# Optimization experiments

Measured on AMD Instinct MI355X. Metric: run time of the kernel, lower is better.

## Reference

```python
import jax, jax.numpy as jnp
import numpy as np

# dims
B, N, T, F, D = 16, 64, 168, 8, 248   # batch, stations, seq, features, gcn_dim
E = D + F                              # transformer dmodel = 256
H = 8                                  # attention heads
FF = 4 * E                             # expansion_factor * dmodel


def _layer_norm(x, g, b, eps=1e-5):
    m = jnp.mean(x, axis=-1, keepdims=True)
    v = jnp.var(x, axis=-1, keepdims=True)
    return (x - m) * jax.lax.rsqrt(v + eps) * g + b


def setup_inputs() -> dict:
    key = jax.random.key(0)
    ks = jax.random.split(key, 20)
    s = 0.02
    return {
        'x': jax.random.normal(ks[0], (B, N, T, F), jnp.float32),
        'locs': jax.random.uniform(ks[1], (B, N, 2), jnp.float32),
        'pos_em': jax.random.normal(ks[2], (B, T, E), jnp.float32),
        'periodic_em': jax.random.normal(ks[3], (B, T, E), jnp.float32),
        'gcn_w': jax.random.normal(ks[4], (F, D), jnp.float32) * s,
        'gcn_b': jnp.zeros((D,), jnp.float32),
        'fc1_w': jax.random.normal(ks[5], (D, D), jnp.float32) * s,
        'fc1_b': jnp.zeros((D,), jnp.float32),
        'wq': jax.random.normal(ks[6], (E, E), jnp.float32) * s,
        'bq': jnp.zeros((E,), jnp.float32),
        'wk': jax.random.normal(ks[7], (E, E), jnp.float32) * s,
        'bk': jnp.zeros((E,), jnp.float32),
        'wv': jax.random.normal(ks[8], (E, E), jnp.float32) * s,
        'bv': jnp.zeros((E,), jnp.float32),
        'wo': jax.random.normal(ks[9], (E, E), jnp.float32) * s,
        'bo': jnp.zeros((E,), jnp.float32),
        'ln1_g': jnp.ones((E,), jnp.float32),
        'ln1_b': jnp.zeros((E,), jnp.float32),
        'ln2_g': jnp.ones((E,), jnp.float32),
        'ln2_b': jnp.zeros((E,), jnp.float32),
        'ff1_w': jax.random.normal(ks[10], (E, FF), jnp.float32) * s,
        'ff1_b': jnp.zeros((FF,), jnp.float32),
        'ff2_w': jax.random.normal(ks[11], (FF, E), jnp.float32) * s,
        'ff2_b': jnp.zeros((E,), jnp.float32),
    }


def reference(x, locs, pos_em, periodic_em, gcn_w, gcn_b, fc1_w, fc1_b,
              wq, bq, wk, bk, wv, bv, wo, bo,
              ln1_g, ln1_b, ln2_g, ln2_b, ff1_w, ff1_b, ff2_w, ff2_b):
    b, n, t, f = x.shape
    # --- inverse-distance-weighted dense adjacency (fully connected graph) ---
    diff = locs[:, :, None, :] - locs[:, None, :, :]            # [B,N,N,2]
    dist = jnp.sqrt(jnp.sum(diff * diff, -1) + 1e-12)           # [B,N,N]
    w = jnp.where(jnp.eye(n, dtype=bool), 0.0, 1.0 / dist)      # no self edges
    w = w / jnp.sum(w, -1, keepdims=True)                       # norm=True
    # --- GCNConv (self loops + symmetric normalization), batched over B and T ---
    a = w + jnp.eye(n, dtype=x.dtype)
    dinv = jax.lax.rsqrt(jnp.sum(a, -1))
    a = a * dinv[:, :, None] * dinv[:, None, :]                 # [B,N,N]
    h = jnp.einsum('bntf,fd->bntd', x, gcn_w)                   # xW
    g = jax.nn.relu(jnp.einsum('bmn,bntd->bmtd', a, h) + gcn_b) # aggregate + relu
    g = jnp.einsum('bntd,de->bnte', g, fc1_w) + fc1_b           # fc1
    # --- concat features, flatten stations into batch, add positional embedding ---
    tok = jnp.concatenate([x, g], -1).reshape(b * n, t, -1)     # [B*N,T,E]
    tok = tok + jnp.repeat(pos_em, n, axis=0)                   # dropout=identity (eval)
    per = jnp.repeat(periodic_em, n, axis=0)
    # --- transformer encoder layer (periodic embedding conditions Q/K) ---
    e = tok.shape[-1]
    dh = e // H
    qk_in = tok + per
    q = (qk_in @ wq + bq).reshape(b * n, t, H, dh)
    k = (qk_in @ wk + bk).reshape(b * n, t, H, dh)
    v = (tok @ wv + bv).reshape(b * n, t, H, dh)
    s = jnp.einsum('bthd,bshd->bhts', q, k) * (1.0 / float(np.sqrt(dh)))
    p = jax.nn.softmax(s, axis=-1)
    o = jnp.einsum('bhts,bshd->bthd', p, v).reshape(b * n, t, e)
    o = o @ wo + bo
    h1 = _layer_norm(tok + o, ln1_g, ln1_b)
    ff = jax.nn.relu(h1 @ ff1_w + ff1_b) @ ff2_w + ff2_b
    out = _layer_norm(h1 + ff, ln2_g, ln2_b)
    return out.reshape(b, n, t, e)
```

## Files before the change

### kernel.cpp

```cpp
#include <hip/hip_runtime.h>
#include <hip/hip_bf16.h>

constexpr int B_  = 16;
constexpr int N_  = 64;
constexpr int T_  = 168;
constexpr int F_  = 8;
constexpr int E_  = 256;
constexpr int H_  = 8;
constexpr int DH_ = 32;
constexpr int NT_ = N_ * T_;
constexpr int LDQ_ = 768;

typedef __bf16 bf16x8 __attribute__((ext_vector_type(8)));
typedef float  f32x4  __attribute__((ext_vector_type(4)));
typedef float  f32x4u __attribute__((ext_vector_type(4), aligned(4)));

__device__ __forceinline__ unsigned short f2b(float f) {
  union { float f; unsigned int u; } v; v.f = f;
  unsigned int r = (v.u + 0x7FFFu + ((v.u >> 16) & 1u)) >> 16;
  return (unsigned short)r;
}
__device__ __forceinline__ float b2f(unsigned short h) {
  union { unsigned int u; float f; } v; v.u = ((unsigned int)h) << 16;
  return v.f;
}
__device__ __forceinline__ unsigned int cvtpk(float lo, float hi) {
  unsigned int r;
  asm("v_cvt_pk_bf16_f32 %0, %1, %2" : "=v"(r) : "v"(lo), "v"(hi));
  return r;
}
__device__ __forceinline__ void gload16(const void* g, void* l) {
  __builtin_amdgcn_global_load_lds(
      (const __attribute__((address_space(1))) unsigned int*)g,
      (__attribute__((address_space(3))) unsigned int*)l, 16, 0, 0);
}

__global__ void adj_kernel(const float* __restrict__ locs, float* __restrict__ a) {
  int b = blockIdx.x;
  int m = threadIdx.x;
  __shared__ float lx[64], ly[64];
  lx[m] = locs[(b * 64 + m) * 2 + 0];
  ly[m] = locs[(b * 64 + m) * 2 + 1];
  __syncthreads();
  float x = lx[m], y = ly[m];
  float sum = 0.f;
  for (int n = 0; n < 64; ++n) {
    float dx = x - lx[n], dy = y - ly[n];
    float d = sqrtf(dx * dx + dy * dy + 1e-12f);
    sum += (n == m) ? 0.f : 1.f / d;
  }
  float inv = 0.5f / sum;
  for (int n = 0; n < 64; ++n) {
    float dx = x - lx[n], dy = y - ly[n];
    float d = sqrtf(dx * dx + dy * dy + 1e-12f);
    float w = (n == m) ? 0.5f : inv / d;
    a[(b * 64 + m) * 64 + n] = w;
  }
}

__global__ void convw_kernel(const float* __restrict__ in, unsigned short* __restrict__ outT,
                             int K, int N, int Kp, int Np) {
  int idx = blockIdx.x * 256 + threadIdx.x;
  if (idx >= Np * Kp) return;
  int n = idx / Kp, k = idx % Kp;
  float v = (k < K && n < N) ? in[(long)k * N + n] : 0.f;
  outT[idx] = f2b(v);
}

__global__ __launch_bounds__(256) void gcn_kernel(
    const float* __restrict__ x, const float* __restrict__ adj,
    const float* __restrict__ gcn_w, const float* __restrict__ gcn_b,
    const float* __restrict__ pos_em, const float* __restrict__ per_em,
    unsigned short* __restrict__ G, unsigned short* __restrict__ tokb,
    unsigned short* __restrict__ qkb, int b0) {
  int bl = blockIdx.x / T_;
  int t = blockIdx.x % T_;
  int b = b0 + bl;
  int tid = threadIdx.x;
  __shared__ float sX[512];
  __shared__ float sXA[512];
  const float* adjb = adj + b * 4096;
  for (int i = tid; i < 512; i += 256) {
    int n = i >> 3, f = i & 7;
    sX[i] = x[((long)(b * 64 + n) * T_ + t) * F_ + f];
  }
  __syncthreads();
  for (int i = tid; i < 512; i += 256) {
    int m = i >> 3, f = i & 7;
    float s = 0.f;
    for (int n = 0; n < 64; ++n) s += adjb[(m << 6) + n] * sX[(n << 3) + f];
    sXA[i] = s;
  }
  {
    long pbase = ((long)bl * T_ + t) * E_;
    for (int i = tid; i < 512; i += 256) {
      int m = i >> 3, f = i & 7;
      long lrow = (long)(bl * 64 + m) * T_ + t;
      float base = sX[i] + pos_em[pbase + f];
      tokb[lrow * E_ + f] = f2b(base);
      qkb[lrow * E_ + f]  = f2b(base + per_em[pbase + f]);
    }
  }
  __syncthreads();
  for (int i = tid; i < 64 * 256; i += 256) {
    int m = i >> 8, d = i & 255;
    float v = 0.f;
    if (d < 248) {
      float s = gcn_b[d];
      const float* xam = &sXA[m << 3];
#pragma unroll
      for (int f = 0; f < 8; ++f) s += xam[f] * gcn_w[f * 248 + d];
      v = fmaxf(s, 0.f);
    }
    long lrow = (long)(bl * 64 + m) * T_ + t;
    G[lrow * 256 + d] = f2b(v);
  }
}

template <int KCHUNKS, int WAVES>
__global__ __launch_bounds__(WAVES * 64) void block_gemm(
    const unsigned short* __restrict__ A, int lda,
    const unsigned short* __restrict__ Bt, int K, int Nact,
    const float* __restrict__ bias,
    float* Cf, unsigned short* Cb1, unsigned short* Cb2,
    const float* __restrict__ emb1, const float* __restrict__ emb2,
    const unsigned short* __restrict__ resb, const float* resf,
    int c0, int ldc, int relu) {
  __shared__ unsigned short As[64 * 256];
  const int tid = threadIdx.x;
  const int lane = tid & 63, w = tid >> 6;
  const int l15 = lane & 15, lg = lane >> 4;
  const int m0 = blockIdx.x * 64;
  const int n0w = blockIdx.y * (WAVES * 64) + w * 64;

  f32x4 acc[4][4];
#pragma unroll
  for (int i = 0; i < 4; ++i)
#pragma unroll
    for (int j = 0; j < 4; ++j) acc[i][j] = (f32x4){0.f, 0.f, 0.f, 0.f};

  for (int kc = 0; kc < KCHUNKS; ++kc) {
    if (kc) __syncthreads();
#pragma unroll
    for (int j = 0; j < 32 / WAVES; ++j) {
      int idx = j * (WAVES * 64) + tid;
      int row = idx >> 5, g = idx & 31;
      int swg = (g & 24) | ((g & 7) ^ (row & 7));
      gload16(A + (long)(m0 + row) * lda + kc * 256 + swg * 8,
              &As[(j * (WAVES * 64) + w * 64) * 8]);
    }
    bf16x8 Wa[4], Wb[4], Xf[4];
    auto ldw = [&](bf16x8 (&W)[4], int ks) {
#pragma unroll
      for (int nf = 0; nf < 4; ++nf)
        W[nf] = *reinterpret_cast<const bf16x8*>(
            Bt + (long)(n0w + nf * 16 + l15) * K + kc * 256 + ks * 32 + (lg << 3));
    };
    auto ldx = [&](int ks) {
#pragma unroll
      for (int mf = 0; mf < 4; ++mf) {
        int row = (mf << 4) + l15;
        int ksg = (ks << 2) + lg;
        int sw = (ksg & 24) | ((ksg & 7) ^ (row & 7));
        Xf[mf] = *reinterpret_cast<const bf16x8*>(&As[((row << 5) + sw) * 8]);
      }
    };
    auto mm = [&](bf16x8 (&W)[4]) {
      __builtin_amdgcn_s_setprio(1);
#pragma unroll
      for (int mf = 0; mf < 4; ++mf)
#pragma unroll
        for (int nf = 0; nf < 4; ++nf)
          acc[mf][nf] = __builtin_amdgcn_mfma_f32_16x16x32_bf16(W[nf], Xf[mf], acc[mf][nf], 0, 0, 0);
      __builtin_amdgcn_s_setprio(0);
    };
    ldw(Wa, 0);
    asm volatile("s_waitcnt vmcnt(0)" ::: "memory");
    __syncthreads();
#pragma unroll
    for (int kp = 0; kp < 4; ++kp) {
      ldw(Wb, kp * 2 + 1);
      ldx(kp * 2);
      mm(Wa);
      if (kp < 3) ldw(Wa, kp * 2 + 2);
      ldx(kp * 2 + 1);
      mm(Wb);
    }
  }

  const int cb = lg << 2;
#pragma unroll
  for (int mf = 0; mf < 4; ++mf) {
    int rr = m0 + (mf << 4) + l15;
    int ar = (rr / NT_) * T_ + (rr % T_);
    long rbase  = (long)rr * ldc + c0;
    long rbase2 = (long)rr * 256 + c0;
    long abase  = (long)ar * 256 + c0;
#pragma unroll
    for (int nf = 0; nf < 4; ++nf) {
      int gcol = n0w + (nf << 4) + cb;
      if (gcol < Nact) {
        float v0 = acc[mf][nf][0], v1 = acc[mf][nf][1];
        float v2 = acc[mf][nf][2], v3 = acc[mf][nf][3];
        if (bias) {
          f32x4u b4 = *reinterpret_cast<const f32x4u*>(bias + gcol);
          v0 += b4[0]; v1 += b4[1]; v2 += b4[2]; v3 += b4[3];
        }
        if (relu) {
          v0 = fmaxf(v0, 0.f); v1 = fmaxf(v1, 0.f);
          v2 = fmaxf(v2, 0.f); v3 = fmaxf(v3, 0.f);
        }
        if (resb) {
          ushort4 rv = *reinterpret_cast<const ushort4*>(resb + rbase2 + gcol);
          v0 += b2f(rv.x); v1 += b2f(rv.y); v2 += b2f(rv.z); v3 += b2f(rv.w);
        }
        if (resf) {
          f32x4u r4 = *reinterpret_cast<const f32x4u*>(resf + rbase + gcol);
          v0 += r4[0]; v1 += r4[1]; v2 += r4[2]; v3 += r4[3];
        }
        if (emb1) {
          f32x4u e4 = *reinterpret_cast<const f32x4u*>(emb1 + abase + gcol);
          v0 += e4[0]; v1 += e4[1]; v2 += e4[2]; v3 += e4[3];
        }
        if (Cf) {
          f32x4u o; o[0] = v0; o[1] = v1; o[2] = v2; o[3] = v3;
          *reinterpret_cast<f32x4u*>(Cf + rbase + gcol) = o;
        }
        if (Cb1) {
          uint2 p = {cvtpk(v0, v1), cvtpk(v2, v3)};
          *reinterpret_cast<uint2*>(Cb1 + rbase + gcol) = p;
        }
        if (Cb2) {
          f32x4u e4 = *reinterpret_cast<const f32x4u*>(emb2 + abase + gcol);
          uint2 p = {cvtpk(v0 + e4[0], v1 + e4[1]), cvtpk(v2 + e4[2], v3 + e4[3])};
          *reinterpret_cast<uint2*>(Cb2 + rbase + gcol) = p;
        }
      }
    }
  }
}

__global__ __launch_bounds__(256) void wo_ln_kernel(
    const unsigned short* __restrict__ A, int lda,
    const unsigned short* __restrict__ Wt,
    const float* __restrict__ bias,
    const unsigned short* __restrict__ resb,
    const float* __restrict__ lng, const float* __restrict__ lnb,
    unsigned short* __restrict__ outb) {
  __shared__ unsigned short As[64 * 256];
  __shared__ float red[4][4][16][2];
  const int tid = threadIdx.x;
  const int lane = tid & 63, w = tid >> 6;
  const int l15 = lane & 15, lg = lane >> 4;
  const int m0 = blockIdx.x * 64;
  const int n0w = w * 64;

  f32x4 acc[4][4];
#pragma unroll
  for (int i = 0; i < 4; ++i)
#pragma unroll
    for (int j = 0; j < 4; ++j) acc[i][j] = (f32x4){0.f, 0.f, 0.f, 0.f};

#pragma unroll
  for (int j = 0; j < 8; ++j) {
    int idx = j * 256 + tid;
    int row = idx >> 5, g = idx & 31;
    int swg = (g & 24) | ((g & 7) ^ (row & 7));
    gload16(A + (long)(m0 + row) * lda + swg * 8, &As[(j * 256 + w * 64) * 8]);
  }
  bf16x8 Wa[4], Wb[4], Xf[4];
  auto ldw = [&](bf16x8 (&W)[4], int ks) {
#pragma unroll
    for (int nf = 0; nf < 4; ++nf)
      W[nf] = *reinterpret_cast<const bf16x8*>(
          Wt + (long)(n0w + nf * 16 + l15) * 256 + ks * 32 + (lg << 3));
  };
  auto ldx = [&](int ks) {
#pragma unroll
    for (int mf = 0; mf < 4; ++mf) {
      int row = (mf << 4) + l15;
      int ksg = (ks << 2) + lg;
      int sw = (ksg & 24) | ((ksg & 7) ^ (row & 7));
      Xf[mf] = *reinterpret_cast<const bf16x8*>(&As[((row << 5) + sw) * 8]);
    }
  };
  auto mm = [&](bf16x8 (&W)[4]) {
    __builtin_amdgcn_s_setprio(1);
#pragma unroll
    for (int mf = 0; mf < 4; ++mf)
#pragma unroll
      for (int nf = 0; nf < 4; ++nf)
        acc[mf][nf] = __builtin_amdgcn_mfma_f32_16x16x32_bf16(W[nf], Xf[mf], acc[mf][nf], 0, 0, 0);
    __builtin_amdgcn_s_setprio(0);
  };
  ldw(Wa, 0);
  asm volatile("s_waitcnt vmcnt(0)" ::: "memory");
  __syncthreads();
#pragma unroll
  for (int kp = 0; kp < 4; ++kp) {
    ldw(Wb, kp * 2 + 1);
    ldx(kp * 2);
    mm(Wa);
    if (kp < 3) ldw(Wa, kp * 2 + 2);
    ldx(kp * 2 + 1);
    mm(Wb);
  }

  const int cb = lg << 2;
  float s[4], s2[4];
#pragma unroll
  for (int mf = 0; mf < 4; ++mf) {
    int rr = m0 + (mf << 4) + l15;
    long rbase2 = (long)rr * 256;
    s[mf] = 0.f; s2[mf] = 0.f;
#pragma unroll
    for (int nf = 0; nf < 4; ++nf) {
      int gcol = n0w + (nf << 4) + cb;
      f32x4u b4 = *reinterpret_cast<const f32x4u*>(bias + gcol);
      ushort4 rv = *reinterpret_cast<const ushort4*>(resb + rbase2 + gcol);
      float v0 = acc[mf][nf][0] + b4[0] + b2f(rv.x);
      float v1 = acc[mf][nf][1] + b4[1] + b2f(rv.y);
      float v2 = acc[mf][nf][2] + b4[2] + b2f(rv.z);
      float v3 = acc[mf][nf][3] + b4[3] + b2f(rv.w);
      acc[mf][nf][0] = v0; acc[mf][nf][1] = v1;
      acc[mf][nf][2] = v2; acc[mf][nf][3] = v3;
      s[mf] += v0 + v1 + v2 + v3;
      s2[mf] += v0 * v0 + v1 * v1 + v2 * v2 + v3 * v3;
    }
    s[mf] += __shfl_xor(s[mf], 16, 64);
    s[mf] += __shfl_xor(s[mf], 32, 64);
    s2[mf] += __shfl_xor(s2[mf], 16, 64);
    s2[mf] += __shfl_xor(s2[mf], 32, 64);
    if (lg == 0) { red[w][mf][l15][0] = s[mf]; red[w][mf][l15][1] = s2[mf]; }
  }
  __syncthreads();
#pragma unroll
  for (int mf = 0; mf < 4; ++mf) {
    float S  = red[0][mf][l15][0] + red[1][mf][l15][0] + red[2][mf][l15][0] + red[3][mf][l15][0];
    float S2 = red[0][mf][l15][1] + red[1][mf][l15][1] + red[2][mf][l15][1] + red[3][mf][l15][1];
    float mean = S * 0.00390625f;
    float var = S2 * 0.00390625f - mean * mean;
    float rs = rsqrtf(var + 1e-5f);
    int rr = m0 + (mf << 4) + l15;
    long rbase = (long)rr * 256;
#pragma unroll
    for (int nf = 0; nf < 4; ++nf) {
      int gcol = n0w + (nf << 4) + cb;
      f32x4u g4 = *reinterpret_cast<const f32x4u*>(lng + gcol);
      f32x4u t4 = *reinterpret_cast<const f32x4u*>(lnb + gcol);
      float o0 = (acc[mf][nf][0] - mean) * rs * g4[0] + t4[0];
      float o1 = (acc[mf][nf][1] - mean) * rs * g4[1] + t4[1];
      float o2 = (acc[mf][nf][2] - mean) * rs * g4[2] + t4[2];
      float o3 = (acc[mf][nf][3] - mean) * rs * g4[3] + t4[3];
      uint2 p = {cvtpk(o0, o1), cvtpk(o2, o3)};
      *reinterpret_cast<uint2*>(outb + rbase + gcol) = p;
    }
  }
}

__global__ __launch_bounds__(512, 4) void ff_fused_kernel(
    const unsigned short* __restrict__ h1,
    const unsigned short* __restrict__ W1,
    const unsigned short* __restrict__ W2,
    const float* __restrict__ b1, const float* __restrict__ b2,
    const float* __restrict__ lng, const float* __restrict__ lnb,
    float* __restrict__ out) {
  __shared__ unsigned short h1s[64 * 256];
  __shared__ unsigned short fisA[64 * 128];
  __shared__ unsigned short fisB[64 * 128];
  __shared__ float red[8][4][16][2];
  const int tid = threadIdx.x;
  const int lane = tid & 63, w = tid >> 6;
  const int l15 = lane & 15, lg = lane >> 4;
  const int m0 = blockIdx.x * 64;
  const int cb = lg << 2;

#pragma unroll
  for (int j = 0; j < 4; ++j) {
    int idx = j * 512 + tid;
    int row = idx >> 5, g = idx & 31;
    int swg = (g & 24) | ((g & 7) ^ (row & 7));
    gload16(h1 + (long)(m0 + row) * 256 + swg * 8, &h1s[(j * 512 + w * 64) * 8]);
  }
  asm volatile("s_waitcnt vmcnt(0)" ::: "memory");
  __syncthreads();

  f32x4 acc2[4][2];
#pragma unroll
  for (int i = 0; i < 4; ++i)
#pragma unroll
    for (int j = 0; j < 2; ++j) acc2[i][j] = (f32x4){0.f, 0.f, 0.f, 0.f};

  auto ldw1 = [&](bf16x8& W, int hc, int ks) {
    W = *reinterpret_cast<const bf16x8*>(
        W1 + (long)(hc * 128 + w * 16 + l15) * 256 + ks * 32 + (lg << 3));
  };
  auto stage1 = [&](f32x4 (&a1)[4], int hc) {
#pragma unroll
    for (int i = 0; i < 4; ++i) a1[i] = (f32x4){0.f, 0.f, 0.f, 0.f};
    bf16x8 Wa, Wb, Xf[4];
    auto ldxh = [&](int ks) {
#pragma unroll
      for (int mf = 0; mf < 4; ++mf) {
        int row = (mf << 4) + l15;
        int ksg = (ks << 2) + lg;
        int sw = (ksg & 24) | ((ksg & 7) ^ (row & 7));
        Xf[mf] = *reinterpret_cast<const bf16x8*>(&h1s[((row << 5) + sw) * 8]);
      }
    };
    ldw1(Wa, hc, 0);
#pragma unroll
    for (int kp = 0; kp < 4; ++kp) {
      ldw1(Wb, hc, kp * 2 + 1);
      ldxh(kp * 2);
      __builtin_amdgcn_s_setprio(1);
#pragma unroll
      for (int mf = 0; mf < 4; ++mf)
        a1[mf] = __builtin_amdgcn_mfma_f32_16x16x32_bf16(Wa, Xf[mf], a1[mf], 0, 0, 0);
      __builtin_amdgcn_s_setprio(0);
      if (kp < 3) ldw1(Wa, hc, kp * 2 + 2);
      ldxh(kp * 2 + 1);
      __builtin_amdgcn_s_setprio(1);
#pragma unroll
      for (int mf = 0; mf < 4; ++mf)
        a1[mf] = __builtin_amdgcn_mfma_f32_16x16x32_bf16(Wb, Xf[mf], a1[mf], 0, 0, 0);
      __builtin_amdgcn_s_setprio(0);
    }
  };
  auto stage2 = [&](const unsigned short* fis, int hc) {
    bf16x8 Wf[2], Xf[4];
#pragma unroll
    for (int ks = 0; ks < 4; ++ks) {
#pragma unroll
      for (int nf = 0; nf < 2; ++nf)
        Wf[nf] = *reinterpret_cast<const bf16x8*>(
            W2 + (long)(w * 32 + nf * 16 + l15) * 1024 + hc * 128 + ks * 32 + (lg << 3));
#pragma unroll
      for (int mf = 0; mf < 4; ++mf) {
        int row = (mf << 4) + l15;
        int ksg = (ks << 2) + lg;
        int sw = (ksg & 8) | ((ksg & 7) ^ (row & 7));
        Xf[mf] = *reinterpret_cast<const bf16x8*>(&fis[((row << 4) + sw) * 8]);
      }
      __builtin_amdgcn_s_setprio(1);
#pragma unroll
      for (int mf = 0; mf < 4; ++mf)
#pragma unroll
        for (int nf = 0; nf < 2; ++nf)
          acc2[mf][nf] = __builtin_amdgcn_mfma_f32_16x16x32_bf16(Wf[nf], Xf[mf], acc2[mf][nf], 0, 0, 0);
      __builtin_amdgcn_s_setprio(0);
    }
  };
  auto writeFis = [&](unsigned short* fis, f32x4 (&a1)[4], int hc) {
    int col = w * 16 + cb;
    f32x4u b4 = *reinterpret_cast<const f32x4u*>(b1 + hc * 128 + col);
    int g = col >> 3;
#pragma unroll
    for (int mf = 0; mf < 4; ++mf) {
      int row = (mf << 4) + l15;
      float v0 = fmaxf(a1[mf][0] + b4[0], 0.f);
      float v1 = fmaxf(a1[mf][1] + b4[1], 0.f);
      float v2 = fmaxf(a1[mf][2] + b4[2], 0.f);
      float v3 = fmaxf(a1[mf][3] + b4[3], 0.f);
      int swg = (g & 8) | ((g & 7) ^ (row & 7));
      uint2 p = {cvtpk(v0, v1), cvtpk(v2, v3)};
      *reinterpret_cast<uint2*>(&fis[((row << 4) + swg) * 8 + (col & 7)]) = p;
    }
  };

  f32x4 a1[4];
  stage1(a1, 0);
  writeFis(fisA, a1, 0);
  __syncthreads();

#pragma unroll
  for (int hc = 0; hc < 8; ++hc) {
    const unsigned short* rdp = (hc & 1) ? fisB : fisA;
    unsigned short* wrp = (hc & 1) ? fisA : fisB;
    if (hc < 7) stage1(a1, hc + 1);
    stage2(rdp, hc);
    if (hc < 7) {
      writeFis(wrp, a1, hc + 1);
      __syncthreads();
    }
  }

  float s[4], s2[4];
#pragma unroll
  for (int mf = 0; mf < 4; ++mf) {
    int row = (mf << 4) + l15;
    s[mf] = 0.f; s2[mf] = 0.f;
#pragma unroll
    for (int nf = 0; nf < 2; ++nf) {
      int gcol = w * 32 + (nf << 4) + cb;
      f32x4u b4 = *reinterpret_cast<const f32x4u*>(b2 + gcol);
      int g = gcol >> 3;
      int swg = (g & 24) | ((g & 7) ^ (row & 7));
      ushort4 rv = *reinterpret_cast<const ushort4*>(&h1s[((row << 5) + swg) * 8 + (gcol & 7)]);
      float v0 = acc2[mf][nf][0] + b4[0] + b2f(rv.x);
      float v1 = acc2[mf][nf][1] + b4[1] + b2f(rv.y);
      float v2 = acc2[mf][nf][2] + b4[2] + b2f(rv.z);
      float v3 = acc2[mf][nf][3] + b4[3] + b2f(rv.w);
      acc2[mf][nf][0] = v0; acc2[mf][nf][1] = v1;
      acc2[mf][nf][2] = v2; acc2[mf][nf][3] = v3;
      s[mf] += v0 + v1 + v2 + v3;
      s2[mf] += v0 * v0 + v1 * v1 + v2 * v2 + v3 * v3;
    }
    s[mf] += __shfl_xor(s[mf], 16, 64);
    s[mf] += __shfl_xor(s[mf], 32, 64);
    s2[mf] += __shfl_xor(s2[mf], 16, 64);
    s2[mf] += __shfl_xor(s2[mf], 32, 64);
    if (lg == 0) { red[w][mf][l15][0] = s[mf]; red[w][mf][l15][1] = s2[mf]; }
  }
  __syncthreads();
#pragma unroll
  for (int mf = 0; mf < 4; ++mf) {
    float S = 0.f, S2 = 0.f;
#pragma unroll
    for (int ww = 0; ww < 8; ++ww) { S += red[ww][mf][l15][0]; S2 += red[ww][mf][l15][1]; }
    float mean = S * 0.00390625f;
    float var = S2 * 0.00390625f - mean * mean;
    float rs = rsqrtf(var + 1e-5f);
    int rr = m0 + (mf << 4) + l15;
    long rbase = (long)rr * 256;
#pragma unroll
    for (int nf = 0; nf < 2; ++nf) {
      int gcol = w * 32 + (nf << 4) + cb;
      f32x4u g4 = *reinterpret_cast<const f32x4u*>(lng + gcol);
      f32x4u t4 = *reinterpret_cast<const f32x4u*>(lnb + gcol);
      f32x4u o;
      o[0] = (acc2[mf][nf][0] - mean) * rs * g4[0] + t4[0];
      o[1] = (acc2[mf][nf][1] - mean) * rs * g4[1] + t4[1];
      o[2] = (acc2[mf][nf][2] - mean) * rs * g4[2] + t4[2];
      o[3] = (acc2[mf][nf][3] - mean) * rs * g4[3] + t4[3];
      *reinterpret_cast<f32x4u*>(out + rbase + gcol) = o;
    }
  }
}

__global__ __launch_bounds__(256) void attn_mfma_kernel(unsigned short* QKV) {
  int blk = blockIdx.x;
  int bn = blk >> 3, h = blk & 7;
  int tid = threadIdx.x;
  int lane = tid & 63, w = tid >> 6;

  __shared__ unsigned short Kfr[11 * 512];
  __shared__ unsigned short VT[32][200];
  __shared__ unsigned short Pb[4][16][200];

  const long qbase = (long)bn * T_ * LDQ_ + h * DH_;
  const unsigned short* Kg = QKV + qbase + 256;
  const unsigned short* V  = QKV + qbase + 512;
  const unsigned short* Q  = QKV + qbase;
  unsigned short* O = QKV + qbase;
  int l15 = lane & 15, lg = lane >> 4;

  for (int kt = w; kt < 11; kt += 4) {
    gload16(Kg + (long)(kt * 16 + l15) * LDQ_ + (lg << 3), &Kfr[kt * 512]);
  }
  for (int i = tid; i < T_ * 4; i += 256) {
    int t = i >> 2, seg = (i & 3) << 3;
    uint4 vv = *reinterpret_cast<const uint4*>(V + (long)t * LDQ_ + seg);
    const unsigned short* vs = (const unsigned short*)&vv;
#pragma unroll
    for (int j = 0; j < 8; ++j) VT[seg + j][t] = vs[j];
  }
  for (int i = tid; i < 32 * 32; i += 256) VT[i >> 5][168 + (i & 31)] = 0;
  {
    unsigned short* pflat = &Pb[0][0][0];
    for (int i = tid; i < 64 * 24; i += 256)
      pflat[(i / 24) * 200 + 176 + (i % 24)] = 0;
  }
  __syncthreads();

  const float scale = 0.17677669529663687f;
  unsigned short* Pw = &Pb[w][0][0];

  for (int it = 0; it < 3; ++it) {
    int qt = w + it * 4;
    if (qt > 10) break;
    bf16x8 af = *reinterpret_cast<const bf16x8*>(
        Q + (long)(qt * 16 + l15) * LDQ_ + (lg << 3));
    f32x4 s[11];
#pragma unroll
    for (int kt = 0; kt < 11; ++kt) {
      bf16x8 bf = *reinterpret_cast<const bf16x8*>(&Kfr[kt * 512 + lane * 8]);
      s[kt] = __builtin_amdgcn_mfma_f32_16x16x32_bf16(
          af, bf, (f32x4){0.f, 0.f, 0.f, 0.f}, 0, 0, 0);
    }
    bool ok10 = (l15 < 8);
    float inv_l[4];
#pragma unroll
    for (int r = 0; r < 4; ++r) {
      float mx = -1e30f;
#pragma unroll
      for (int kt = 0; kt < 10; ++kt) mx = fmaxf(mx, s[kt][r] * scale);
      if (ok10) mx = fmaxf(mx, s[10][r] * scale);
#pragma unroll
      for (int off = 1; off < 16; off <<= 1) mx = fmaxf(mx, __shfl_xor(mx, off, 64));
      float pv[11];
      float ls = 0.f;
#pragma unroll
      for (int kt = 0; kt < 11; ++kt) {
        bool valid = (kt < 10) || ok10;
        float p = valid ? __expf(s[kt][r] * scale - mx) : 0.f;
        pv[kt] = p;
        ls += p;
      }
#pragma unroll
      for (int off = 1; off < 16; off <<= 1) ls += __shfl_xor(ls, off, 64);
      inv_l[r] = 1.f / ls;
      int prow = (lg << 2) + r;
#pragma unroll
      for (int kt = 0; kt < 11; ++kt)
        Pw[prow * 200 + kt * 16 + l15] = f2b(pv[kt]);
    }
    asm volatile("s_waitcnt lgkmcnt(0)" ::: "memory");
    __builtin_amdgcn_sched_barrier(0);
    f32x4 o0 = (f32x4){0.f, 0.f, 0.f, 0.f};
    f32x4 o1 = (f32x4){0.f, 0.f, 0.f, 0.f};
#pragma unroll
    for (int ks = 0; ks < 6; ++ks) {
      bf16x8 pf = *reinterpret_cast<const bf16x8*>(&Pw[l15 * 200 + ks * 32 + (lg << 3)]);
      bf16x8 v0 = *reinterpret_cast<const bf16x8*>(&VT[l15][ks * 32 + (lg << 3)]);
      bf16x8 v1 = *reinterpret_cast<const bf16x8*>(&VT[16 + l15][ks * 32 + (lg << 3)]);
      o0 = __builtin_amdgcn_mfma_f32_16x16x32_bf16(pf, v0, o0, 0, 0, 0);
      o1 = __builtin_amdgcn_mfma_f32_16x16x32_bf16(pf, v1, o1, 0, 0, 0);
    }
    int rg = lg << 2;
#pragma unroll
    for (int r = 0; r < 4; ++r) {
      int q = qt * 16 + rg + r;
      if (q < T_) {
        long ob = (long)q * LDQ_;
        O[ob + l15]      = f2b(o0[r] * inv_l[r]);
        O[ob + 16 + l15] = f2b(o1[r] * inv_l[r]);
      }
    }
  }
}

extern "C" void kernel_launch(void* const* d_in, const int* in_sizes, int n_in,
                              void* d_out, int out_size, void* d_ws, size_t ws_size,
                              hipStream_t stream) {
  const float* x      = (const float*)d_in[0];
  const float* locs   = (const float*)d_in[1];
  const float* pos_em = (const float*)d_in[2];
  const float* per_em = (const float*)d_in[3];
  const float* gcn_w  = (const float*)d_in[4];
  const float* gcn_b  = (const float*)d_in[5];
  const float* fc1_w  = (const float*)d_in[6];
  const float* fc1_b  = (const float*)d_in[7];
  const float* wq = (const float*)d_in[8];
  const float* bq = (const float*)d_in[9];
  const float* wk = (const float*)d_in[10];
  const float* bk = (const float*)d_in[11];
  const float* wv = (const float*)d_in[12];
  const float* bv = (const float*)d_in[13];
  const float* wo = (const float*)d_in[14];
  const float* bo = (const float*)d_in[15];
  const float* ln1_g = (const float*)d_in[16];
  const float* ln1_b = (const float*)d_in[17];
  const float* ln2_g = (const float*)d_in[18];
  const float* ln2_b = (const float*)d_in[19];
  const float* ff1_w = (const float*)d_in[20];
  const float* ff1_b = (const float*)d_in[21];
  const float* ff2_w = (const float*)d_in[22];
  const float* ff2_b = (const float*)d_in[23];
  float* out = (float*)d_out;

  const size_t ADJ_BYTES = 1u << 20;
  const size_t WB_BYTES  = 2u << 20;
  int CB = 16;
  while (CB > 1) {
    if (ADJ_BYTES + WB_BYTES + (size_t)CB * NT_ * 2560 <= ws_size) break;
    CB >>= 1;
  }
  char* ws = (char*)d_ws;
  float* adj = (float*)ws;
  unsigned short* wslab = (unsigned short*)(ws + ADJ_BYTES);
  unsigned short* fc1T  = wslab;
  unsigned short* wqkT  = wslab + 65536;
  unsigned short* wkT   = wslab + 2 * 65536;
  unsigned short* wvT   = wslab + 3 * 65536;
  unsigned short* woT   = wslab + 4 * 65536;
  unsigned short* ff1T  = wslab + 5 * 65536;
  unsigned short* ff2T  = wslab + 5 * 65536 + 262144;
  float* bqk = (float*)(ws + ADJ_BYTES + 1900544);

  unsigned short* tokb = (unsigned short*)(ws + ADJ_BYTES + WB_BYTES);
  unsigned short* qkb  = tokb + (size_t)CB * NT_ * 256;
  unsigned short* qkv  = qkb + (size_t)CB * NT_ * 256;
  unsigned short* h1b  = tokb;

  adj_kernel<<<B_, 64, 0, stream>>>(locs, adj);
  convw_kernel<<<256, 256, 0, stream>>>(fc1_w, fc1T, 248, 248, 256, 256);
  convw_kernel<<<256, 256, 0, stream>>>(wq, wqkT, 256, 256, 256, 256);
  convw_kernel<<<256, 256, 0, stream>>>(wk, wkT, 256, 256, 256, 256);
  convw_kernel<<<256, 256, 0, stream>>>(wv, wvT, 256, 256, 256, 256);
  convw_kernel<<<256, 256, 0, stream>>>(wo, woT, 256, 256, 256, 256);
  convw_kernel<<<1024, 256, 0, stream>>>(ff1_w, ff1T, 256, 1024, 256, 1024);
  convw_kernel<<<1024, 256, 0, stream>>>(ff2_w, ff2T, 1024, 256, 1024, 256);
  hipMemcpyAsync(bqk, bq, 256 * sizeof(float), hipMemcpyDeviceToDevice, stream);
  hipMemcpyAsync(bqk + 256, bk, 256 * sizeof(float), hipMemcpyDeviceToDevice, stream);

  for (int b0 = 0; b0 < B_; b0 += CB) {
    const int rows = CB * NT_;
    const int GX = rows / 64;
    const float* pos_c = pos_em + (long)b0 * T_ * E_;
    const float* per_c = per_em + (long)b0 * T_ * E_;
    float* out_c = out + (long)b0 * NT_ * E_;
    unsigned short* G = qkv;

    gcn_kernel<<<CB * T_, 256, 0, stream>>>(x, adj, gcn_w, gcn_b, pos_c, per_c,
                                            G, tokb, qkb, b0);
    block_gemm<1, 4><<<dim3(GX, 1), 256, 0, stream>>>(
        G, 256, fc1T, 256, 248, fc1_b, nullptr, tokb, qkb, pos_c, per_c,
        nullptr, nullptr, 8, 256, 0);
    block_gemm<1, 8><<<dim3(GX, 1), 512, 0, stream>>>(
        qkb, 256, wqkT, 256, 512, bqk, nullptr, qkv, nullptr, nullptr, nullptr,
        nullptr, nullptr, 0, LDQ_, 0);
    block_gemm<1, 4><<<dim3(GX, 1), 256, 0, stream>>>(
        tokb, 256, wvT, 256, 256, bv, nullptr, qkv, nullptr, nullptr, nullptr,
        nullptr, nullptr, 512, LDQ_, 0);
    attn_mfma_kernel<<<CB * N_ * H_, 256, 0, stream>>>(qkv);
    wo_ln_kernel<<<GX, 256, 0, stream>>>(qkv, LDQ_, woT, bo, tokb,
                                         ln1_g, ln1_b, h1b);
    ff_fused_kernel<<<GX, 512, 0, stream>>>(h1b, ff1T, ff2T, ff1_b, ff2_b,
                                            ln2_g, ln2_b, out_c);
  }
}
```

Before: 1.173 ms.

## Restructure fused FFN to single fis buffer with register-prefetched W1/W2 weights

```diff
diff --git a/kernel.cpp b/kernel.cpp
--- a/kernel.cpp
+++ b/kernel.cpp
@@ -366,8 +366,7 @@
     const float* __restrict__ lng, const float* __restrict__ lnb,
     float* __restrict__ out) {
   __shared__ unsigned short h1s[64 * 256];
-  __shared__ unsigned short fisA[64 * 128];
-  __shared__ unsigned short fisB[64 * 128];
+  __shared__ unsigned short fis[64 * 128];
   __shared__ float red[8][4][16][2];
   const int tid = threadIdx.x;
   const int lane = tid & 63, w = tid >> 6;
@@ -382,8 +381,6 @@
     int swg = (g & 24) | ((g & 7) ^ (row & 7));
     gload16(h1 + (long)(m0 + row) * 256 + swg * 8, &h1s[(j * 512 + w * 64) * 8]);
   }
-  asm volatile("s_waitcnt vmcnt(0)" ::: "memory");
-  __syncthreads();
 
   f32x4 acc2[4][2];
 #pragma unroll
@@ -391,98 +388,97 @@
 #pragma unroll
     for (int j = 0; j < 2; ++j) acc2[i][j] = (f32x4){0.f, 0.f, 0.f, 0.f};
 
+  bf16x8 W1all[8], W2A[2], W2B[2], Xf[4];
   auto ldw1 = [&](bf16x8& W, int hc, int ks) {
     W = *reinterpret_cast<const bf16x8*>(
         W1 + (long)(hc * 128 + w * 16 + l15) * 256 + ks * 32 + (lg << 3));
   };
-  auto stage1 = [&](f32x4 (&a1)[4], int hc) {
+  auto ldw2 = [&](bf16x8 (&W)[2], int hc, int ks) {
+#pragma unroll
+    for (int nf = 0; nf < 2; ++nf)
+      W[nf] = *reinterpret_cast<const bf16x8*>(
+          W2 + (long)(w * 32 + nf * 16 + l15) * 1024 + hc * 128 + ks * 32 + (lg << 3));
+  };
+  auto ldxh = [&](int ks) {
+#pragma unroll
+    for (int mf = 0; mf < 4; ++mf) {
+      int row = (mf << 4) + l15;
+      int ksg = (ks << 2) + lg;
+      int sw = (ksg & 24) | ((ksg & 7) ^ (row & 7));
+      Xf[mf] = *reinterpret_cast<const bf16x8*>(&h1s[((row << 5) + sw) * 8]);
+    }
+  };
+  auto ldxf = [&](int ks) {
+#pragma unroll
+    for (int mf = 0; mf < 4; ++mf) {
+      int row = (mf << 4) + l15;
+      int ksg = (ks << 2) + lg;
+      int sw = (ksg & 8) | ((ksg & 7) ^ (row & 7));
+      Xf[mf] = *reinterpret_cast<const bf16x8*>(&fis[((row << 4) + sw) * 8]);
+    }
+  };
+  auto mm2 = [&](bf16x8 (&W)[2]) {
+    __builtin_amdgcn_s_setprio(1);
+#pragma unroll
+    for (int mf = 0; mf < 4; ++mf)
+#pragma unroll
+      for (int nf = 0; nf < 2; ++nf)
+        acc2[mf][nf] = __builtin_amdgcn_mfma_f32_16x16x32_bf16(W[nf], Xf[mf], acc2[mf][nf], 0, 0, 0);
+    __builtin_amdgcn_s_setprio(0);
+  };
+
+#pragma unroll
+  for (int ks = 0; ks < 8; ++ks) ldw1(W1all[ks], 0, ks);
+  asm volatile("s_waitcnt vmcnt(8)" ::: "memory");
+  __syncthreads();
+
+  for (int hc = 0; hc < 8; ++hc) {
+    f32x4 a1[4];
 #pragma unroll
     for (int i = 0; i < 4; ++i) a1[i] = (f32x4){0.f, 0.f, 0.f, 0.f};
-    bf16x8 Wa, Wb, Xf[4];
-    auto ldxh = [&](int ks) {
+    ldw2(W2A, hc, 0);
+    ldw2(W2B, hc, 1);
+#pragma unroll
+    for (int ks = 0; ks < 8; ++ks) {
+      ldxh(ks);
+      __builtin_amdgcn_s_setprio(1);
+#pragma unroll
+      for (int mf = 0; mf < 4; ++mf)
+        a1[mf] = __builtin_amdgcn_mfma_f32_16x16x32_bf16(W1all[ks], Xf[mf], a1[mf], 0, 0, 0);
+      __builtin_amdgcn_s_setprio(0);
+    }
+    if (hc) __syncthreads();
+    {
+      int col = w * 16 + cb;
+      f32x4u b4 = *reinterpret_cast<const f32x4u*>(b1 + hc * 128 + col);
+      int g = col >> 3;
 #pragma unroll
       for (int mf = 0; mf < 4; ++mf) {
         int row = (mf << 4) + l15;
-        int ksg = (ks << 2) + lg;
-        int sw = (ksg & 24) | ((ksg & 7) ^ (row & 7));
-        Xf[mf] = *reinterpret_cast<const bf16x8*>(&h1s[((row << 5) + sw) * 8]);
+        float v0 = fmaxf(a1[mf][0] + b4[0], 0.f);
+        float v1 = fmaxf(a1[mf][1] + b4[1], 0.f);
+        float v2 = fmaxf(a1[mf][2] + b4[2], 0.f);
+        float v3 = fmaxf(a1[mf][3] + b4[3], 0.f);
+        int swg = (g & 8) | ((g & 7) ^ (row & 7));
+        uint2 p = {cvtpk(v0, v1), cvtpk(v2, v3)};
+        *reinterpret_cast<uint2*>(&fis[((row << 4) + swg) * 8 + (col & 7)]) = p;
       }
-    };
-    ldw1(Wa, hc, 0);
-#pragma unroll
-    for (int kp = 0; kp < 4; ++kp) {
-      ldw1(Wb, hc, kp * 2 + 1);
-      ldxh(kp * 2);
-      __builtin_amdgcn_s_setprio(1);
-#pragma unroll
-      for (int mf = 0; mf < 4; ++mf)
-        a1[mf] = __builtin_amdgcn_mfma_f32_16x16x32_bf16(Wa, Xf[mf], a1[mf], 0, 0, 0);
-      __builtin_amdgcn_s_setprio(0);
-      if (kp < 3) ldw1(Wa, hc, kp * 2 + 2);
-      ldxh(kp * 2 + 1);
-      __builtin_amdgcn_s_setprio(1);
-#pragma unroll
-      for (int mf = 0; mf < 4; ++mf)
-        a1[mf] = __builtin_amdgcn_mfma_f32_16x16x32_bf16(Wb, Xf[mf], a1[mf], 0, 0, 0);
-      __builtin_amdgcn_s_setprio(0);
-    }
-  };
-  auto stage2 = [&](const unsigned short* fis, int hc) {
-    bf16x8 Wf[2], Xf[4];
-#pragma unroll
-    for (int ks = 0; ks < 4; ++ks) {
-#pragma unroll
-      for (int nf = 0; nf < 2; ++nf)
-        Wf[nf] = *reinterpret_cast<const bf16x8*>(
-            W2 + (long)(w * 32 + nf * 16 + l15) * 1024 + hc * 128 + ks * 32 + (lg << 3));
-#pragma unroll
-      for (int mf = 0; mf < 4; ++mf) {
-        int row = (mf << 4) + l15;
-        int ksg = (ks << 2) + lg;
-        int sw = (ksg & 8) | ((ksg & 7) ^ (row & 7));
-        Xf[mf] = *reinterpret_cast<const bf16x8*>(&fis[((row << 4) + sw) * 8]);
-      }
-      __builtin_amdgcn_s_setprio(1);
-#pragma unroll
-      for (int mf = 0; mf < 4; ++mf)
-#pragma unroll
-        for (int nf = 0; nf < 2; ++nf)
-          acc2[mf][nf] = __builtin_amdgcn_mfma_f32_16x16x32_bf16(Wf[nf], Xf[mf], acc2[mf][nf], 0, 0, 0);
-      __builtin_amdgcn_s_setprio(0);
-    }
-  };
-  auto writeFis = [&](unsigned short* fis, f32x4 (&a1)[4], int hc) {
-    int col = w * 16 + cb;
-    f32x4u b4 = *reinterpret_cast<const f32x4u*>(b1 + hc * 128 + col);
-    int g = col >> 3;
-#pragma unroll
-    for (int mf = 0; mf < 4; ++mf) {
-      int row = (mf << 4) + l15;
-      float v0 = fmaxf(a1[mf][0] + b4[0], 0.f);
-      float v1 = fmaxf(a1[mf][1] + b4[1], 0.f);
-      float v2 = fmaxf(a1[mf][2] + b4[2], 0.f);
-      float v3 = fmaxf(a1[mf][3] + b4[3], 0.f);
-      int swg = (g & 8) | ((g & 7) ^ (row & 7));
-      uint2 p = {cvtpk(v0, v1), cvtpk(v2, v3)};
-      *reinterpret_cast<uint2*>(&fis[((row << 4) + swg) * 8 + (col & 7)]) = p;
-    }
-  };
-
-  f32x4 a1[4];
-  stage1(a1, 0);
-  writeFis(fisA, a1, 0);
-  __syncthreads();
-
-#pragma unroll
-  for (int hc = 0; hc < 8; ++hc) {
-    const unsigned short* rdp = (hc & 1) ? fisB : fisA;
-    unsigned short* wrp = (hc & 1) ? fisA : fisB;
-    if (hc < 7) stage1(a1, hc + 1);
-    stage2(rdp, hc);
+    }
+    __syncthreads();
+    ldxf(0);
+    mm2(W2A);
+    ldw2(W2A, hc, 2);
     if (hc < 7) {
-      writeFis(wrp, a1, hc + 1);
-      __syncthreads();
-    }
+#pragma unroll
+      for (int k2 = 0; k2 < 8; ++k2) ldw1(W1all[k2], hc + 1, k2);
+    }
+    ldxf(1);
+    mm2(W2B);
+    ldw2(W2B, hc, 3);
+    ldxf(2);
+    mm2(W2A);
+    ldxf(3);
+    mm2(W2B);
   }
 
   float s[4], s2[4];
```

After: 1.543 ms. 31.6% more time.
